# Optimization experiments

Hardware: AMD Instinct MI355X
Metric: run time of the kernel (lower is better)

## Reference

```python
import jax, jax.numpy as jnp
import numpy as np

HIDDEN = 2048
NUM_EXPERTS = 64
TOP_K = 8
EPS = 1e-6


def setup_inputs() -> dict:
    key = jax.random.key(0)
    k1, k2, k3, k4 = jax.random.split(key, 4)
    hidden_states = jax.random.normal(k1, (4, 4096, HIDDEN), dtype=jnp.float32)
    scale = jnp.ones((HIDDEN,), dtype=jnp.float32) + 0.01 * jax.random.normal(k2, (HIDDEN,), dtype=jnp.float32)
    proj_w = jax.random.normal(k3, (NUM_EXPERTS, HIDDEN), dtype=jnp.float32) * (HIDDEN ** -0.5)
    per_expert_scale = jnp.ones((NUM_EXPERTS,), dtype=jnp.float32) + 0.01 * jax.random.normal(k4, (NUM_EXPERTS,), dtype=jnp.float32)
    return {"hidden_states": hidden_states, "scale": scale, "proj_w": proj_w, "per_expert_scale": per_expert_scale}


def reference(hidden_states, scale, proj_w, per_expert_scale):
    H = hidden_states.shape[-1]
    # RMSNorm without learned scale
    x = hidden_states * jax.lax.rsqrt(jnp.mean(hidden_states * hidden_states, axis=-1, keepdims=True) + EPS)
    # elementwise scale and 1/sqrt(H) root-size scaling
    x = x * scale * (H ** -0.5)
    # router logits: [B,S,E]
    logits = jnp.einsum("bsh,eh->bse", x, proj_w)
    router_probs = jax.nn.softmax(logits.astype(jnp.float32), axis=-1)
    top_k_weights, top_k_index = jax.lax.top_k(router_probs, TOP_K)
    top_k_weights = top_k_weights / jnp.sum(top_k_weights, axis=-1, keepdims=True)
    top_k_weights = top_k_weights * per_expert_scale[top_k_index]
    # histc with bins=E, min=0, max=E on integer indices == bincount
    num_tokens_per_expert = jnp.bincount(top_k_index.reshape(-1), length=NUM_EXPERTS).astype(jnp.float32)
    return (top_k_weights.astype(hidden_states.dtype), top_k_index, num_tokens_per_expert)
```

## Files before the change

kernel.cpp:

```cpp
#include <hip/hip_runtime.h>
#include <math.h>

#define HIDDEN   2048
#define NEXPERT  64
#define TOPK     8
#define NTOK     16384
#define TOKB     16
#define RSQRT_H  0.02209708691207961
#define WSCALE   64.0f

typedef __attribute__((ext_vector_type(8))) _Float16       v8h;
typedef __attribute__((ext_vector_type(8))) unsigned short v8u;
typedef __attribute__((ext_vector_type(4))) float          v4f;

static __device__ __forceinline__ unsigned short f16b(float x) {
    return __builtin_bit_cast(unsigned short, (_Float16)x);
}
static __device__ __forceinline__ float f16f(unsigned short u) {
    return (float)__builtin_bit_cast(_Float16, u);
}

__global__ __launch_bounds__(256) void prep_wf(
    const float* __restrict__ w, const float* __restrict__ scale,
    unsigned short* __restrict__ wf, float* __restrict__ out_c)
{
    int i    = blockIdx.x * 256 + threadIdx.x;
    if (i < NEXPERT) out_c[i] = 0.f;
    int j    = i & 7;
    int lane = (i >> 3) & 63;
    int nt   = (i >> 9) & 3;
    int ks   = i >> 11;
    int e    = nt * 16 + (lane & 15);
    int k    = ks * 32 + (lane >> 4) * 8 + j;
    float v  = w[e * HIDDEN + k] * scale[k] * WSCALE;
    unsigned short vh = f16b(v);
    unsigned short vl = f16b(v - f16f(vh));
    size_t base = (((size_t)(ks * 4 + nt) * 2) * 64 + lane) * 8 + j;
    wf[base]       = vh;
    wf[base + 512] = vl;
}

static __device__ __forceinline__ void cvt8(
    float4 a, float4 b, v8h& ah, v8h& al, float& ss)
{
    float vv[8] = {a.x, a.y, a.z, a.w, b.x, b.y, b.z, b.w};
    v8u uh, ul;
#pragma unroll
    for (int j = 0; j < 8; ++j) {
        float v = vv[j];
        unsigned short hh = f16b(v);
        uh[j] = hh;
        ul[j] = f16b(v - f16f(hh));
        ss    = fmaf(v, v, ss);
    }
    ah = __builtin_bit_cast(v8h, uh);
    al = __builtin_bit_cast(v8h, ul);
}

__global__ __launch_bounds__(256, 4) void router_main(
    const float* __restrict__ h, const unsigned short* __restrict__ wf,
    const float* __restrict__ pes,
    float* __restrict__ out_w, float* __restrict__ out_i, float* __restrict__ out_c)
{
    __shared__ __align__(16) float lg[4 * 16 * 65];
    __shared__ float lss[4 * 16];
    __shared__ int   hist[NEXPERT];

    const int tid  = (int)threadIdx.x;
    const int w    = __builtin_amdgcn_readfirstlane(tid >> 6);
    const int lane = tid & 63;
    const int m    = lane & 15;
    const int quad = lane >> 4;
    const int t0   = (int)blockIdx.x * TOKB;

    if (tid < NEXPERT) hist[tid] = 0;

    const float* xp = h + (size_t)(t0 + m) * HIDDEN + w * 512 + quad * 8;
    const unsigned short* wq = wf + (size_t)(w * 16) * 4096 + (size_t)lane * 8;

    v4f acc[4];
#pragma unroll
    for (int nt = 0; nt < 4; ++nt) acc[nt] = (v4f)0.f;
    float ss = 0.f;

    float4 xa = *(const float4*)xp;
    float4 xb = *(const float4*)(xp + 4);

#pragma unroll
    for (int s = 0; s < 16; ++s) {
        const unsigned short* bq = wq + (size_t)s * 4096;
        v8h bh[4], bl[4];
#pragma unroll
        for (int nt = 0; nt < 4; ++nt) {
            bh[nt] = *(const v8h*)(bq + nt * 1024);
            bl[nt] = *(const v8h*)(bq + nt * 1024 + 512);
        }
        float4 na, nb;
        if (s < 15) {
            na = *(const float4*)(xp + (s + 1) * 32);
            nb = *(const float4*)(xp + (s + 1) * 32 + 4);
        }
        __builtin_amdgcn_sched_barrier(0);

        v8h ah, al;
        cvt8(xa, xb, ah, al, ss);
#pragma unroll
        for (int nt = 0; nt < 4; ++nt) {
            acc[nt] = __builtin_amdgcn_mfma_f32_16x16x32_f16(ah, bh[nt], acc[nt], 0, 0, 0);
            acc[nt] = __builtin_amdgcn_mfma_f32_16x16x32_f16(ah, bl[nt], acc[nt], 0, 0, 0);
            acc[nt] = __builtin_amdgcn_mfma_f32_16x16x32_f16(al, bh[nt], acc[nt], 0, 0, 0);
        }

        if (s < 15) { xa = na; xb = nb; }
    }

    {
        float s = ss;
        s += __shfl_xor(s, 16, 64);
        s += __shfl_xor(s, 32, 64);
        if (lane < 16) lss[w * 16 + lane] = s;
    }

#pragma unroll
    for (int nt = 0; nt < 4; ++nt)
#pragma unroll
        for (int r = 0; r < 4; ++r)
            lg[(w * 16 + quad * 4 + r) * 65 + nt * 16 + m] = acc[nt][r];
    __syncthreads();

    for (int i = 0; i < 4; ++i) {
        const int tok = w * 4 + i;
        float lsum = (lg[tok * 65 + lane]        + lg[1040 + tok * 65 + lane])
                   + (lg[2080 + tok * 65 + lane] + lg[3120 + tok * 65 + lane]);
        float sst4 = (lss[tok] + lss[16 + tok]) + (lss[32 + tok] + lss[48 + tok]);
        double sst = (double)sst4;
        double rr  = 1.0 / sqrt(sst * (1.0 / (double)HIDDEN) + 1e-6);
        float logit = (float)((double)lsum * rr * (RSQRT_H / (double)WSCALE));

        float work = logit;
        float myval = 0.f; int myidx = 0; float m0 = 0.f;
#pragma unroll
        for (int j = 0; j < TOPK; ++j) {
            float mx = work;
#pragma unroll
            for (int off = 32; off; off >>= 1) mx = fmaxf(mx, __shfl_xor(mx, off, 64));
            unsigned long long msk = __ballot(work == mx);
            int src = __ffsll((long long)msk) - 1;
            if (j == 0) m0 = mx;
            if (lane == j) { myval = mx; myidx = src; }
            if (lane == src) work = -3.402823466e38f;
        }

        float ev = (lane < TOPK) ? expf(myval - m0) : 0.f;
        float es = ev;
        es += __shfl_xor(es, 1, 64);
        es += __shfl_xor(es, 2, 64);
        es += __shfl_xor(es, 4, 64);
        if (lane < TOPK) {
            float wgt = (ev / es) * pes[myidx];
            size_t o = (size_t)(t0 + tok) * TOPK + lane;
            out_w[o] = wgt;
            out_i[o] = (float)myidx;
            atomicAdd(&hist[myidx], 1);
        }
    }

    __syncthreads();
    if (tid < NEXPERT)
        atomicAdd(&out_c[tid], (float)hist[tid]);
}

extern "C" void kernel_launch(void* const* d_in, const int* in_sizes, int n_in,
                              void* d_out, int out_size, void* d_ws, size_t ws_size,
                              hipStream_t stream) {
    const float* h     = (const float*)d_in[0];
    const float* scale = (const float*)d_in[1];
    const float* w     = (const float*)d_in[2];
    const float* pes   = (const float*)d_in[3];

    unsigned short* wf = (unsigned short*)d_ws;

    float* out_w = (float*)d_out;
    float* out_i = (float*)d_out + (size_t)NTOK * TOPK;
    float* out_c = (float*)d_out + (size_t)NTOK * TOPK * 2;

    prep_wf<<<512, 256, 0, stream>>>(w, scale, wf, out_c);

    router_main<<<NTOK / TOKB, 256, 0, stream>>>(h, wf, pes, out_w, out_i, out_c);
}
```

Measured before the change: 226.4 us.

## Process 32 tokens per block to reuse weight fragments across two MFMA tiles

Each block now handles two 16-token tiles, so every weight fragment loaded from global memory feeds two sets of MFMAs. This halves weight traffic per token and halves the grid size. Activation loads become nontemporal to avoid polluting cache. The cost is more registers for two accumulator sets and double-buffered prefetches, which may lower occupancy under the 4-wave launch bound, plus more LDS.

```diff
diff --git a/kernel.cpp b/kernel.cpp
--- a/kernel.cpp
+++ b/kernel.cpp
@@ -5,7 +5,7 @@
 #define NEXPERT  64
 #define TOPK     8
 #define NTOK     16384
-#define TOKB     16
+#define TOKB     32
 #define RSQRT_H  0.02209708691207961
 #define WSCALE   64.0f
 
@@ -41,9 +41,9 @@
 }
 
 static __device__ __forceinline__ void cvt8(
-    float4 a, float4 b, v8h& ah, v8h& al, float& ss)
+    v4f a, v4f b, v8h& ah, v8h& al, float& ss)
 {
-    float vv[8] = {a.x, a.y, a.z, a.w, b.x, b.y, b.z, b.w};
+    float vv[8] = {a[0], a[1], a[2], a[3], b[0], b[1], b[2], b[3]};
     v8u uh, ul;
 #pragma unroll
     for (int j = 0; j < 8; ++j) {
@@ -62,8 +62,8 @@
     const float* __restrict__ pes,
     float* __restrict__ out_w, float* __restrict__ out_i, float* __restrict__ out_c)
 {
-    __shared__ __align__(16) float lg[4 * 16 * 65];
-    __shared__ float lss[4 * 16];
+    __shared__ __align__(16) float lg[4 * 32 * 66];
+    __shared__ float lss[4 * 32];
     __shared__ int   hist[NEXPERT];
 
     const int tid  = (int)threadIdx.x;
@@ -75,16 +75,19 @@
 
     if (tid < NEXPERT) hist[tid] = 0;
 
-    const float* xp = h + (size_t)(t0 + m) * HIDDEN + w * 512 + quad * 8;
+    const float* xp0 = h + (size_t)(t0 + m) * HIDDEN + w * 512 + quad * 8;
+    const float* xp1 = xp0 + (size_t)16 * HIDDEN;
     const unsigned short* wq = wf + (size_t)(w * 16) * 4096 + (size_t)lane * 8;
 
-    v4f acc[4];
-#pragma unroll
-    for (int nt = 0; nt < 4; ++nt) acc[nt] = (v4f)0.f;
-    float ss = 0.f;
-
-    float4 xa = *(const float4*)xp;
-    float4 xb = *(const float4*)(xp + 4);
+    v4f acc0[4], acc1[4];
+#pragma unroll
+    for (int nt = 0; nt < 4; ++nt) { acc0[nt] = (v4f)0.f; acc1[nt] = (v4f)0.f; }
+    float ss0 = 0.f, ss1 = 0.f;
+
+    v4f xa0 = __builtin_nontemporal_load((const v4f*)xp0);
+    v4f xb0 = __builtin_nontemporal_load((const v4f*)(xp0 + 4));
+    v4f xa1 = __builtin_nontemporal_load((const v4f*)xp1);
+    v4f xb1 = __builtin_nontemporal_load((const v4f*)(xp1 + 4));
 
 #pragma unroll
     for (int s = 0; s < 16; ++s) {
@@ -95,44 +98,63 @@
             bh[nt] = *(const v8h*)(bq + nt * 1024);
             bl[nt] = *(const v8h*)(bq + nt * 1024 + 512);
         }
-        float4 na, nb;
+        v4f na0, nb0, na1, nb1;
         if (s < 15) {
-            na = *(const float4*)(xp + (s + 1) * 32);
-            nb = *(const float4*)(xp + (s + 1) * 32 + 4);
+            na0 = __builtin_nontemporal_load((const v4f*)(xp0 + (s + 1) * 32));
+            nb0 = __builtin_nontemporal_load((const v4f*)(xp0 + (s + 1) * 32 + 4));
+            na1 = __builtin_nontemporal_load((const v4f*)(xp1 + (s + 1) * 32));
+            nb1 = __builtin_nontemporal_load((const v4f*)(xp1 + (s + 1) * 32 + 4));
         }
         __builtin_amdgcn_sched_barrier(0);
 
-        v8h ah, al;
-        cvt8(xa, xb, ah, al, ss);
-#pragma unroll
-        for (int nt = 0; nt < 4; ++nt) {
-            acc[nt] = __builtin_amdgcn_mfma_f32_16x16x32_f16(ah, bh[nt], acc[nt], 0, 0, 0);
-            acc[nt] = __builtin_amdgcn_mfma_f32_16x16x32_f16(ah, bl[nt], acc[nt], 0, 0, 0);
-            acc[nt] = __builtin_amdgcn_mfma_f32_16x16x32_f16(al, bh[nt], acc[nt], 0, 0, 0);
-        }
-
-        if (s < 15) { xa = na; xb = nb; }
+        {
+            v8h ah, al;
+            cvt8(xa0, xb0, ah, al, ss0);
+#pragma unroll
+            for (int nt = 0; nt < 4; ++nt) {
+                acc0[nt] = __builtin_amdgcn_mfma_f32_16x16x32_f16(ah, bh[nt], acc0[nt], 0, 0, 0);
+                acc0[nt] = __builtin_amdgcn_mfma_f32_16x16x32_f16(ah, bl[nt], acc0[nt], 0, 0, 0);
+                acc0[nt] = __builtin_amdgcn_mfma_f32_16x16x32_f16(al, bh[nt], acc0[nt], 0, 0, 0);
+            }
+        }
+        {
+            v8h ah, al;
+            cvt8(xa1, xb1, ah, al, ss1);
+#pragma unroll
+            for (int nt = 0; nt < 4; ++nt) {
+                acc1[nt] = __builtin_amdgcn_mfma_f32_16x16x32_f16(ah, bh[nt], acc1[nt], 0, 0, 0);
+                acc1[nt] = __builtin_amdgcn_mfma_f32_16x16x32_f16(ah, bl[nt], acc1[nt], 0, 0, 0);
+                acc1[nt] = __builtin_amdgcn_mfma_f32_16x16x32_f16(al, bh[nt], acc1[nt], 0, 0, 0);
+            }
+        }
+
+        if (s < 15) { xa0 = na0; xb0 = nb0; xa1 = na1; xb1 = nb1; }
     }
 
     {
-        float s = ss;
-        s += __shfl_xor(s, 16, 64);
-        s += __shfl_xor(s, 32, 64);
-        if (lane < 16) lss[w * 16 + lane] = s;
+        float s0 = ss0, s1 = ss1;
+        s0 += __shfl_xor(s0, 16, 64); s0 += __shfl_xor(s0, 32, 64);
+        s1 += __shfl_xor(s1, 16, 64); s1 += __shfl_xor(s1, 32, 64);
+        if (lane < 16) {
+            lss[w * 32 + lane]      = s0;
+            lss[w * 32 + 16 + lane] = s1;
+        }
     }
 
 #pragma unroll
     for (int nt = 0; nt < 4; ++nt)
 #pragma unroll
-        for (int r = 0; r < 4; ++r)
-            lg[(w * 16 + quad * 4 + r) * 65 + nt * 16 + m] = acc[nt][r];
+        for (int r = 0; r < 4; ++r) {
+            lg[(w * 32 + quad * 4 + r) * 66 + nt * 16 + m]      = acc0[nt][r];
+            lg[(w * 32 + 16 + quad * 4 + r) * 66 + nt * 16 + m] = acc1[nt][r];
+        }
     __syncthreads();
 
-    for (int i = 0; i < 4; ++i) {
-        const int tok = w * 4 + i;
-        float lsum = (lg[tok * 65 + lane]        + lg[1040 + tok * 65 + lane])
-                   + (lg[2080 + tok * 65 + lane] + lg[3120 + tok * 65 + lane]);
-        float sst4 = (lss[tok] + lss[16 + tok]) + (lss[32 + tok] + lss[48 + tok]);
+    for (int i = 0; i < 8; ++i) {
+        const int tok = w * 8 + i;
+        float lsum = (lg[(0 * 32 + tok) * 66 + lane] + lg[(1 * 32 + tok) * 66 + lane])
+                   + (lg[(2 * 32 + tok) * 66 + lane] + lg[(3 * 32 + tok) * 66 + lane]);
+        float sst4 = (lss[tok] + lss[32 + tok]) + (lss[64 + tok] + lss[96 + tok]);
         double sst = (double)sst4;
         double rr  = 1.0 / sqrt(sst * (1.0 / (double)HIDDEN) + 1e-6);
         float logit = (float)((double)lsum * rr * (RSQRT_H / (double)WSCALE));
```

Result: faster. 221.2 us (-2.3%).
